# Optimization experiments

Measured on AMD Instinct MI355X. Metric: run time of the kernel, lower is better.

## Reference

```python
import jax, jax.numpy as jnp
from jax import lax
import numpy as np

C_IN, C_OUT, K, STRIDE, PAD = 64, 64, 3, 1, 1
EPS = 1e-5


def setup_inputs() -> dict:
    key = jax.random.key(0)
    ks = jax.random.split(key, 6)
    B, H, W = 4, 128, 128
    x = jax.random.normal(ks[0], (B, C_IN, H, W), jnp.float32)
    # small offset weights -> realistic sub-pixel offsets
    offset_w = jax.random.normal(ks[1], (2 * K * K, C_IN, K, K), jnp.float32) * 0.01
    offset_b = jax.random.normal(ks[2], (2 * K * K,), jnp.float32) * 0.01
    dcn_w = jax.random.normal(ks[3], (C_OUT, C_IN, K, K), jnp.float32) / np.sqrt(C_IN * K * K)
    gamma = jax.random.uniform(ks[4], (C_OUT,), jnp.float32, 0.5, 1.5)
    beta = jax.random.normal(ks[5], (C_OUT,), jnp.float32) * 0.1
    return dict(x=x, offset_w=offset_w, offset_b=offset_b, dcn_w=dcn_w, gamma=gamma, beta=beta)


def _bilinear_sample(xb, py, px):
    # xb: (C,H,W); py,px: (K2,Ho,Wo) absolute sample coords (may be out of bounds)
    H, W = xb.shape[1], xb.shape[2]
    y0 = jnp.floor(py); x0 = jnp.floor(px)
    wy = py - y0  # frac weights
    wx = px - x0

    def gather(yi, xi):
        yc = jnp.clip(yi, 0, H - 1).astype(jnp.int32)
        xc = jnp.clip(xi, 0, W - 1).astype(jnp.int32)
        v = xb[:, yc, xc]  # (C,K2,Ho,Wo)
        valid = ((yi >= 0) & (yi <= H - 1) & (xi >= 0) & (xi <= W - 1)).astype(xb.dtype)
        return v * valid[None]

    return (gather(y0, x0) * ((1 - wy) * (1 - wx))[None]
            + gather(y0, x0 + 1) * ((1 - wy) * wx)[None]
            + gather(y0 + 1, x0) * (wy * (1 - wx))[None]
            + gather(y0 + 1, x0 + 1) * (wy * wx)[None])  # (C,K2,Ho,Wo)


def reference(x, offset_w, offset_b, dcn_w, gamma, beta):
    B, C, H, W = x.shape
    K2 = K * K
    # offset conv (standard conv, NCHW)
    offset = lax.conv_general_dilated(
        x, offset_w, (STRIDE, STRIDE), [(PAD, PAD), (PAD, PAD)],
        dimension_numbers=("NCHW", "OIHW", "NCHW")) + offset_b[None, :, None, None]
    Ho, Wo = offset.shape[2], offset.shape[3]
    off = offset.reshape(B, K2, 2, Ho, Wo)  # interleaved (dy, dx) per tap
    dy, dx = off[:, :, 0], off[:, :, 1]
    # base sampling grid: out_pos*stride - pad + kernel tap index
    hs = (jnp.arange(Ho) * STRIDE - PAD).astype(x.dtype)
    ws = (jnp.arange(Wo) * STRIDE - PAD).astype(x.dtype)
    ki, kj = jnp.meshgrid(jnp.arange(K), jnp.arange(K), indexing="ij")
    ki = ki.reshape(K2).astype(x.dtype)
    kj = kj.reshape(K2).astype(x.dtype)
    py = dy + hs[None, None, :, None] + ki[None, :, None, None]  # (B,K2,Ho,Wo)
    px = dx + ws[None, None, None, :] + kj[None, :, None, None]

    sampled = jax.vmap(_bilinear_sample)(x, py, px)  # (B,C,K2,Ho,Wo)
    out = jnp.einsum("bckhw,ock->bohw", sampled, dcn_w.reshape(dcn_w.shape[0], C, K2))

    # BatchNorm (training-mode batch stats) + ReLU
    mean = out.mean((0, 2, 3))
    var = out.var((0, 2, 3))
    out = (out - mean[None, :, None, None]) * lax.rsqrt(var + EPS)[None, :, None, None]
    out = out * gamma[None, :, None, None] + beta[None, :, None, None]
    return jnp.maximum(out, 0.0)
```

## Files before the change

kernel.cpp:

```cpp
#include <hip/hip_runtime.h>

#define HW   16384
#define NPX  65536

typedef unsigned short u16;
typedef unsigned int   u32;
typedef short bf16x8 __attribute__((ext_vector_type(8)));
typedef float f32x4  __attribute__((ext_vector_type(4)));

__device__ __forceinline__ u16 f2b(float f) {
    u32 u = __float_as_uint(f);
    return (u16)((u + 0x7FFFu + ((u >> 16) & 1u)) >> 16);
}
__device__ __forceinline__ float blo(u32 u) { return __uint_as_float(u << 16); }
__device__ __forceinline__ float bhi(u32 u) { return __uint_as_float(u & 0xffff0000u); }

__device__ __forceinline__ u32 comb(u32 a00, u32 a01, u32 a10, u32 a11,
                                    float w00, float w01, float w10, float w11) {
    float lo = fmaf(w11, blo(a11), fmaf(w10, blo(a10), fmaf(w01, blo(a01), w00 * blo(a00))));
    float hi = fmaf(w11, bhi(a11), fmaf(w10, bhi(a10), fmaf(w01, bhi(a01), w00 * bhi(a00))));
    return ((__float_as_uint(lo) + 0x8000u) >> 16) | ((__float_as_uint(hi) + 0x8000u) & 0xffff0000u);
}
__device__ __forceinline__ bf16x8 comb4(int4 v00, int4 v01, int4 v10, int4 v11,
                                        float w00, float w01, float w10, float w11) {
    int4 r;
    r.x = comb(v00.x, v01.x, v10.x, v11.x, w00, w01, w10, w11);
    r.y = comb(v00.y, v01.y, v10.y, v11.y, w00, w01, w10, w11);
    r.z = comb(v00.z, v01.z, v10.z, v11.z, w00, w01, w10, w11);
    r.w = comb(v00.w, v01.w, v10.w, v11.w, w00, w01, w10, w11);
    return __builtin_bit_cast(bf16x8, r);
}

#define MFMA __builtin_amdgcn_mfma_f32_16x16x32_bf16

__global__ __launch_bounds__(256)
void k_pre(const float* __restrict__ x, const float* __restrict__ dw,
           const float* __restrict__ ow, u16* __restrict__ xh,
           u16* __restrict__ wtd, u16* __restrict__ wto,
           float* __restrict__ sums) {
    int tid = threadIdx.x;
    int bid = blockIdx.x;
    if (bid >= 512) {
        if (bid == 539) {
            for (int i = tid; i < 1024; i += 256) sums[i] = 0.f;
            return;
        }
        int gid = (bid - 512) * 256 + tid;
        if (gid >= 108 * 64) return;
        int fid = gid >> 6, lane = gid & 63;
        int mi = lane & 15, quad = lane >> 4;
        u32 w[4];
        if (fid < 72) {
            int tap = fid >> 3, rem = fid & 7;
            int ks = rem >> 2, nt = rem & 3;
            int n = nt * 16 + mi;
            int cb = ks * 32 + quad * 8;
#pragma unroll
            for (int i = 0; i < 4; ++i) {
                u32 lo = f2b(dw[(n * 64 + cb + 2 * i) * 9 + tap]);
                u32 hi = f2b(dw[(n * 64 + cb + 2 * i + 1) * 9 + tap]);
                w[i] = lo | (hi << 16);
            }
            *((int4*)wtd + (fid << 6) + lane) = make_int4(w[0], w[1], w[2], w[3]);
        } else {
            int f2 = fid - 72;
            int tap = f2 >> 2, rem = f2 & 3;
            int ks = rem >> 1, nt = rem & 1;
            int n = nt * 16 + mi;
            int cb = ks * 32 + quad * 8;
#pragma unroll
            for (int i = 0; i < 4; ++i) {
                u32 lo = (n < 18) ? f2b(ow[(n * 64 + cb + 2 * i) * 9 + tap]) : 0u;
                u32 hi = (n < 18) ? f2b(ow[(n * 64 + cb + 2 * i + 1) * 9 + tap]) : 0u;
                w[i] = lo | (hi << 16);
            }
            *((int4*)wto + (f2 << 6) + lane) = make_int4(w[0], w[1], w[2], w[3]);
        }
        return;
    }
    __shared__ u16 tile[64][138];
    int p0  = bid * 128;
    int b   = p0 >> 14;
    int hw0 = p0 & (HW - 1);
    int pxq = (tid & 31) * 4;
    int rr  = tid >> 5;
    const float* src = x + (size_t)b * 64 * HW + hw0 + pxq;
#pragma unroll
    for (int i = 0; i < 8; ++i) {
        int c = i * 8 + rr;
        float4 v = *(const float4*)(src + (size_t)c * HW);
        ushort4 h;
        h.x = f2b(v.x); h.y = f2b(v.y); h.z = f2b(v.z); h.w = f2b(v.w);
        *(ushort4*)&tile[c][pxq] = h;
    }
    __syncthreads();
    int sub = tid & 3;
#pragma unroll
    for (int j = 0; j < 2; ++j) {
        int px = j * 64 + (tid >> 2);
        u32 w[8];
#pragma unroll
        for (int t = 0; t < 8; ++t) {
            int c = sub * 16 + 2 * t;
            w[t] = (u32)tile[c][px] | ((u32)tile[c + 1][px] << 16);
        }
        u16* dst = xh + (size_t)(p0 + px) * 64 + sub * 16;
        *(int4*)dst       = make_int4(w[0], w[1], w[2], w[3]);
        *(int4*)(dst + 8) = make_int4(w[4], w[5], w[6], w[7]);
    }
}

__global__ __launch_bounds__(256, 4)
void k_main(const u16* __restrict__ xh, const u16* __restrict__ wto,
            const u16* __restrict__ wtd, const float* __restrict__ ob,
            float* __restrict__ out, float* __restrict__ sums) {
    __shared__ float offs[2][18][34];
    __shared__ float so[64][33];

    int tid = threadIdx.x;
    int vb  = (blockIdx.x & 7) * 256 + (blockIdx.x >> 3);
    int p0  = vb * 32;
    int b   = p0 >> 14;
    int hw0 = p0 & (HW - 1);
    int y   = hw0 >> 7;
    int x0  = hw0 & 127;
    int wave = tid >> 6, lane = tid & 63;
    int mi = lane & 15, quad = lane >> 4;
    int ks = wave >> 1;
    int m0 = (wave & 1) << 4;
    int xcol = x0 + m0 + mi;
    int koff = ks * 32 + quad * 8;
    const u16* xb = xh + (size_t)b * HW * 64;
    const bf16x8* WO = (const bf16x8*)wto;
    const bf16x8* WD = (const bf16x8*)wtd;

    int4 av[9];
#pragma unroll
    for (int tap = 0; tap < 9; ++tap) {
        int yy = y + tap / 3 - 1;
        int xx = xcol + tap % 3 - 1;
        int yc = min(max(yy, 0), 127), xc = min(max(xx, 0), 127);
        int4 a = *(const int4*)(xb + ((yc << 7) + xc) * 64 + koff);
        if (!(((unsigned)yy < 128u) && ((unsigned)xx < 128u)))
            a = make_int4(0, 0, 0, 0);
        av[tap] = a;
    }
    f32x4 oa0 = {0.f, 0.f, 0.f, 0.f}, oa1 = {0.f, 0.f, 0.f, 0.f};
#pragma unroll
    for (int tap = 0; tap < 9; ++tap) {
        bf16x8 af = __builtin_bit_cast(bf16x8, av[tap]);
        oa0 = MFMA(af, WO[((tap * 4 + ks * 2 + 0) << 6) + lane], oa0, 0, 0, 0);
        oa1 = MFMA(af, WO[((tap * 4 + ks * 2 + 1) << 6) + lane], oa1, 0, 0, 0);
    }
    {
        float bias0 = (ks == 0) ? ob[mi] : 0.f;
#pragma unroll
        for (int r = 0; r < 4; ++r)
            offs[ks][mi][m0 + quad * 4 + r] = oa0[r] + bias0;
        if (mi < 2) {
            float bias1 = (ks == 0) ? ob[16 + mi] : 0.f;
#pragma unroll
            for (int r = 0; r < 4; ++r)
                offs[ks][16 + mi][m0 + quad * 4 + r] = oa1[r] + bias1;
        }
    }
    __syncthreads();

    int pxl = m0 + mi;
    float offv[18];
#pragma unroll
    for (int m = 0; m < 18; ++m)
        offv[m] = offs[0][m][pxl] + offs[1][m][pxl];

    float fy = (float)y, fx = (float)xcol;
    auto coords = [&](int tap, float& w00, float& w01, float& w10, float& w11,
                      int& o00, int& o01, int& o10, int& o11) {
        float py  = offv[2 * tap]     + fy + (float)(tap / 3 - 1);
        float pf  = offv[2 * tap + 1] + fx + (float)(tap % 3 - 1);
        float y0f = floorf(py), x0f = floorf(pf);
        float wy  = py - y0f,   wx  = pf - x0f;
        int   iy0 = (int)y0f,   ix0 = (int)x0f;
        float vy0 = (y0f >=  0.f && y0f <= 127.f) ? 1.f : 0.f;
        float vy1 = (y0f >= -1.f && y0f <= 126.f) ? 1.f : 0.f;
        float vx0 = (x0f >=  0.f && x0f <= 127.f) ? 1.f : 0.f;
        float vx1 = (x0f >= -1.f && x0f <= 126.f) ? 1.f : 0.f;
        int cy0 = min(max(iy0, 0), 127), cy1 = min(max(iy0 + 1, 0), 127);
        int cx0 = min(max(ix0, 0), 127), cx1 = min(max(ix0 + 1, 0), 127);
        w00 = (1.f - wy) * (1.f - wx) * vy0 * vx0;
        w01 = (1.f - wy) * wx * vy0 * vx1;
        w10 = wy * (1.f - wx) * vy1 * vx0;
        w11 = wy * wx * vy1 * vx1;
        o00 = ((cy0 << 7) + cx0) * 64 + koff;
        o01 = ((cy0 << 7) + cx1) * 64 + koff;
        o10 = ((cy1 << 7) + cx0) * 64 + koff;
        o11 = ((cy1 << 7) + cx1) * 64 + koff;
    };

    f32x4 acc0 = {0.f,0.f,0.f,0.f}, acc1 = {0.f,0.f,0.f,0.f};
    f32x4 acc2 = {0.f,0.f,0.f,0.f}, acc3 = {0.f,0.f,0.f,0.f};

    float w00, w01, w10, w11;
    int   o00, o01, o10, o11;
    coords(0, w00, w01, w10, w11, o00, o01, o10, o11);
    int4 v00 = *(const int4*)(xb + o00);
    int4 v01 = *(const int4*)(xb + o01);
    int4 v10 = *(const int4*)(xb + o10);
    int4 v11 = *(const int4*)(xb + o11);
    bf16x8 b0 = WD[((ks * 4 + 0) << 6) + lane];
    bf16x8 b1 = WD[((ks * 4 + 1) << 6) + lane];
    bf16x8 b2 = WD[((ks * 4 + 2) << 6) + lane];
    bf16x8 b3 = WD[((ks * 4 + 3) << 6) + lane];

#pragma unroll
    for (int tap = 0; tap < 9; ++tap) {
        float nw00 = w00, nw01 = w01, nw10 = w10, nw11 = w11;
        int4 nv00 = v00, nv01 = v01, nv10 = v10, nv11 = v11;
        bf16x8 nb0 = b0, nb1 = b1, nb2 = b2, nb3 = b3;
        if (tap < 8) {
            int no00, no01, no10, no11;
            coords(tap + 1, nw00, nw01, nw10, nw11, no00, no01, no10, no11);
            nv00 = *(const int4*)(xb + no00);
            nv01 = *(const int4*)(xb + no01);
            nv10 = *(const int4*)(xb + no10);
            nv11 = *(const int4*)(xb + no11);
            nb0 = WD[(((tap + 1) * 8 + ks * 4 + 0) << 6) + lane];
            nb1 = WD[(((tap + 1) * 8 + ks * 4 + 1) << 6) + lane];
            nb2 = WD[(((tap + 1) * 8 + ks * 4 + 2) << 6) + lane];
            nb3 = WD[(((tap + 1) * 8 + ks * 4 + 3) << 6) + lane];
        }
        __builtin_amdgcn_sched_barrier(0);
        bf16x8 a = comb4(v00, v01, v10, v11, w00, w01, w10, w11);
        acc0 = MFMA(a, b0, acc0, 0, 0, 0);
        acc1 = MFMA(a, b1, acc1, 0, 0, 0);
        acc2 = MFMA(a, b2, acc2, 0, 0, 0);
        acc3 = MFMA(a, b3, acc3, 0, 0, 0);
        w00 = nw00; w01 = nw01; w10 = nw10; w11 = nw11;
        v00 = nv00; v01 = nv01; v10 = nv10; v11 = nv11;
        b0 = nb0; b1 = nb1; b2 = nb2; b3 = nb3;
    }

    if (ks == 1) {
#pragma unroll
        for (int r = 0; r < 4; ++r) {
            so[ 0 + mi][m0 + quad * 4 + r] = acc0[r];
            so[16 + mi][m0 + quad * 4 + r] = acc1[r];
            so[32 + mi][m0 + quad * 4 + r] = acc2[r];
            so[48 + mi][m0 + quad * 4 + r] = acc3[r];
        }
    }
    __syncthreads();
    if (ks == 0) {
#pragma unroll
        for (int r = 0; r < 4; ++r) {
            so[ 0 + mi][m0 + quad * 4 + r] += acc0[r];
            so[16 + mi][m0 + quad * 4 + r] += acc1[r];
            so[32 + mi][m0 + quad * 4 + r] += acc2[r];
            so[48 + mi][m0 + quad * 4 + r] += acc3[r];
        }
    }
    __syncthreads();

    int n  = tid >> 2;
    int c4 = tid & 3;
    int pl = c4 * 8;
    float s = 0.f, q = 0.f;
    float vals[8];
#pragma unroll
    for (int i = 0; i < 8; ++i) {
        float v = so[n][pl + i];
        vals[i] = v;
        s += v;
        q = fmaf(v, v, q);
    }
    float* dst = out + (size_t)(b * 64 + n) * HW + (y << 7) + x0 + pl;
    *(float4*)dst       = make_float4(vals[0], vals[1], vals[2], vals[3]);
    *(float4*)(dst + 4) = make_float4(vals[4], vals[5], vals[6], vals[7]);

    s += __shfl_xor(s, 1); s += __shfl_xor(s, 2);
    q += __shfl_xor(q, 1); q += __shfl_xor(q, 2);
    if (c4 == 0) {
        float* sb = sums + (blockIdx.x & 7) * 128;
        atomicAdd(&sb[n], s);
        atomicAdd(&sb[64 + n], q);
    }
}

__global__ __launch_bounds__(256)
void k_bn(float* __restrict__ out, const float* __restrict__ sums,
          const float* __restrict__ gamma, const float* __restrict__ beta) {
    int i4 = blockIdx.x * 256 + threadIdx.x;
    int e  = i4 << 2;
    int o  = (e >> 14) & 63;
    float sm = 0.f, sq = 0.f;
#pragma unroll
    for (int s8 = 0; s8 < 8; ++s8) {
        sm += sums[s8 * 128 + o];
        sq += sums[s8 * 128 + 64 + o];
    }
    const float n = 65536.f;
    float mean = sm / n;
    float var  = fmaxf(sq / n - mean * mean, 0.f);
    float sc   = rsqrtf(var + 1e-5f) * gamma[o];
    float sh   = beta[o] - mean * sc;
    float4 v = *(const float4*)&out[e];
    v.x = fmaxf(fmaf(v.x, sc, sh), 0.f);
    v.y = fmaxf(fmaf(v.y, sc, sh), 0.f);
    v.z = fmaxf(fmaf(v.z, sc, sh), 0.f);
    v.w = fmaxf(fmaf(v.w, sc, sh), 0.f);
    *(float4*)&out[e] = v;
}

extern "C" void kernel_launch(void* const* d_in, const int* in_sizes, int n_in,
                              void* d_out, int out_size, void* d_ws, size_t ws_size,
                              hipStream_t stream) {
    const float* x     = (const float*)d_in[0];
    const float* ow    = (const float*)d_in[1];
    const float* ob    = (const float*)d_in[2];
    const float* dw    = (const float*)d_in[3];
    const float* gamma = (const float*)d_in[4];
    const float* beta  = (const float*)d_in[5];
    float* out = (float*)d_out;
    char*  wsb = (char*)d_ws;
    u16*   xh   = (u16*)wsb;
    u16*   wtd  = (u16*)(wsb + 8388608);
    u16*   wto  = (u16*)(wsb + 8462336);
    float* sums = (float*)(wsb + 8499200);

    k_pre<<<540, 256, 0, stream>>>(x, dw, ow, xh, wtd, wto, sums);
    k_main<<<2048, 256, 0, stream>>>(xh, wto, wtd, ob, out, sums);
    k_bn<<<4096, 256, 0, stream>>>(out, sums, gamma, beta);
}
```

Baseline: 142.3 us.

## Batch gathers two taps at a time, raise occupancy, use perm for bf16 packing

Replaces the one-tap-ahead software prefetch with batches of two taps: the eight gathers for both taps are issued together, then combined and fed to MFMA. Weight fragments are no longer held in registers ahead of time and are read at their point of use. Launch bounds are raised to five blocks per SM to hide gather latency with more waves, and the two-bf16 pack becomes a single v_perm. The risks are register pressure under the tighter bound, possibly causing spills, and the loss of overlap between a batch's gathers and the previous batch's MFMAs.

```diff
diff --git a/kernel.cpp b/kernel.cpp
--- a/kernel.cpp
+++ b/kernel.cpp
@@ -19,7 +19,8 @@
                                     float w00, float w01, float w10, float w11) {
     float lo = fmaf(w11, blo(a11), fmaf(w10, blo(a10), fmaf(w01, blo(a01), w00 * blo(a00))));
     float hi = fmaf(w11, bhi(a11), fmaf(w10, bhi(a10), fmaf(w01, bhi(a01), w00 * bhi(a00))));
-    return ((__float_as_uint(lo) + 0x8000u) >> 16) | ((__float_as_uint(hi) + 0x8000u) & 0xffff0000u);
+    return __builtin_amdgcn_perm(__float_as_uint(hi) + 0x8000u,
+                                 __float_as_uint(lo) + 0x8000u, 0x07060302u);
 }
 __device__ __forceinline__ bf16x8 comb4(int4 v00, int4 v01, int4 v10, int4 v11,
                                         float w00, float w01, float w10, float w11) {
@@ -110,7 +111,7 @@
     }
 }
 
-__global__ __launch_bounds__(256, 4)
+__global__ __launch_bounds__(256, 5)
 void k_main(const u16* __restrict__ xh, const u16* __restrict__ wto,
             const u16* __restrict__ wtd, const float* __restrict__ ob,
             float* __restrict__ out, float* __restrict__ sums) {
@@ -173,70 +174,53 @@
         offv[m] = offs[0][m][pxl] + offs[1][m][pxl];
 
     float fy = (float)y, fx = (float)xcol;
-    auto coords = [&](int tap, float& w00, float& w01, float& w10, float& w11,
-                      int& o00, int& o01, int& o10, int& o11) {
-        float py  = offv[2 * tap]     + fy + (float)(tap / 3 - 1);
-        float pf  = offv[2 * tap + 1] + fx + (float)(tap % 3 - 1);
-        float y0f = floorf(py), x0f = floorf(pf);
-        float wy  = py - y0f,   wx  = pf - x0f;
-        int   iy0 = (int)y0f,   ix0 = (int)x0f;
-        float vy0 = (y0f >=  0.f && y0f <= 127.f) ? 1.f : 0.f;
-        float vy1 = (y0f >= -1.f && y0f <= 126.f) ? 1.f : 0.f;
-        float vx0 = (x0f >=  0.f && x0f <= 127.f) ? 1.f : 0.f;
-        float vx1 = (x0f >= -1.f && x0f <= 126.f) ? 1.f : 0.f;
-        int cy0 = min(max(iy0, 0), 127), cy1 = min(max(iy0 + 1, 0), 127);
-        int cx0 = min(max(ix0, 0), 127), cx1 = min(max(ix0 + 1, 0), 127);
-        w00 = (1.f - wy) * (1.f - wx) * vy0 * vx0;
-        w01 = (1.f - wy) * wx * vy0 * vx1;
-        w10 = wy * (1.f - wx) * vy1 * vx0;
-        w11 = wy * wx * vy1 * vx1;
-        o00 = ((cy0 << 7) + cx0) * 64 + koff;
-        o01 = ((cy0 << 7) + cx1) * 64 + koff;
-        o10 = ((cy1 << 7) + cx0) * 64 + koff;
-        o11 = ((cy1 << 7) + cx1) * 64 + koff;
-    };
-
     f32x4 acc0 = {0.f,0.f,0.f,0.f}, acc1 = {0.f,0.f,0.f,0.f};
     f32x4 acc2 = {0.f,0.f,0.f,0.f}, acc3 = {0.f,0.f,0.f,0.f};
 
-    float w00, w01, w10, w11;
-    int   o00, o01, o10, o11;
-    coords(0, w00, w01, w10, w11, o00, o01, o10, o11);
-    int4 v00 = *(const int4*)(xb + o00);
-    int4 v01 = *(const int4*)(xb + o01);
-    int4 v10 = *(const int4*)(xb + o10);
-    int4 v11 = *(const int4*)(xb + o11);
-    bf16x8 b0 = WD[((ks * 4 + 0) << 6) + lane];
-    bf16x8 b1 = WD[((ks * 4 + 1) << 6) + lane];
-    bf16x8 b2 = WD[((ks * 4 + 2) << 6) + lane];
-    bf16x8 b3 = WD[((ks * 4 + 3) << 6) + lane];
-
-#pragma unroll
-    for (int tap = 0; tap < 9; ++tap) {
-        float nw00 = w00, nw01 = w01, nw10 = w10, nw11 = w11;
-        int4 nv00 = v00, nv01 = v01, nv10 = v10, nv11 = v11;
-        bf16x8 nb0 = b0, nb1 = b1, nb2 = b2, nb3 = b3;
-        if (tap < 8) {
-            int no00, no01, no10, no11;
-            coords(tap + 1, nw00, nw01, nw10, nw11, no00, no01, no10, no11);
-            nv00 = *(const int4*)(xb + no00);
-            nv01 = *(const int4*)(xb + no01);
-            nv10 = *(const int4*)(xb + no10);
-            nv11 = *(const int4*)(xb + no11);
-            nb0 = WD[(((tap + 1) * 8 + ks * 4 + 0) << 6) + lane];
-            nb1 = WD[(((tap + 1) * 8 + ks * 4 + 1) << 6) + lane];
-            nb2 = WD[(((tap + 1) * 8 + ks * 4 + 2) << 6) + lane];
-            nb3 = WD[(((tap + 1) * 8 + ks * 4 + 3) << 6) + lane];
+#pragma unroll
+    for (int bt = 0; bt < 5; ++bt) {
+        const int ntap = (bt == 4) ? 1 : 2;
+        int4  vv[8];
+        float wts[2][4];
+#pragma unroll
+        for (int j = 0; j < 2; ++j) {
+            if (j < ntap) {
+                int tap = bt * 2 + j;
+                float py  = offv[2 * tap]     + fy + (float)(tap / 3 - 1);
+                float pf  = offv[2 * tap + 1] + fx + (float)(tap % 3 - 1);
+                float y0f = floorf(py), x0f = floorf(pf);
+                float wy  = py - y0f,   wx  = pf - x0f;
+                int   iy0 = (int)y0f,   ix0 = (int)x0f;
+                float vy0 = (y0f >=  0.f && y0f <= 127.f) ? 1.f : 0.f;
+                float vy1 = (y0f >= -1.f && y0f <= 126.f) ? 1.f : 0.f;
+                float vx0 = (x0f >=  0.f && x0f <= 127.f) ? 1.f : 0.f;
+                float vx1 = (x0f >= -1.f && x0f <= 126.f) ? 1.f : 0.f;
+                int cy0 = min(max(iy0, 0), 127), cy1 = min(max(iy0 + 1, 0), 127);
+                int cx0 = min(max(ix0, 0), 127), cx1 = min(max(ix0 + 1, 0), 127);
+                wts[j][0] = (1.f - wy) * (1.f - wx) * vy0 * vx0;
+                wts[j][1] = (1.f - wy) * wx * vy0 * vx1;
+                wts[j][2] = wy * (1.f - wx) * vy1 * vx0;
+                wts[j][3] = wy * wx * vy1 * vx1;
+                vv[j * 4 + 0] = *(const int4*)(xb + ((cy0 << 7) + cx0) * 64 + koff);
+                vv[j * 4 + 1] = *(const int4*)(xb + ((cy0 << 7) + cx1) * 64 + koff);
+                vv[j * 4 + 2] = *(const int4*)(xb + ((cy1 << 7) + cx0) * 64 + koff);
+                vv[j * 4 + 3] = *(const int4*)(xb + ((cy1 << 7) + cx1) * 64 + koff);
+            }
         }
         __builtin_amdgcn_sched_barrier(0);
-        bf16x8 a = comb4(v00, v01, v10, v11, w00, w01, w10, w11);
-        acc0 = MFMA(a, b0, acc0, 0, 0, 0);
-        acc1 = MFMA(a, b1, acc1, 0, 0, 0);
-        acc2 = MFMA(a, b2, acc2, 0, 0, 0);
-        acc3 = MFMA(a, b3, acc3, 0, 0, 0);
-        w00 = nw00; w01 = nw01; w10 = nw10; w11 = nw11;
-        v00 = nv00; v01 = nv01; v10 = nv10; v11 = nv11;
-        b0 = nb0; b1 = nb1; b2 = nb2; b3 = nb3;
+#pragma unroll
+        for (int j = 0; j < 2; ++j) {
+            if (j < ntap) {
+                int tap = bt * 2 + j;
+                bf16x8 a = comb4(vv[j * 4 + 0], vv[j * 4 + 1],
+                                 vv[j * 4 + 2], vv[j * 4 + 3],
+                                 wts[j][0], wts[j][1], wts[j][2], wts[j][3]);
+                acc0 = MFMA(a, WD[((tap * 8 + ks * 4 + 0) << 6) + lane], acc0, 0, 0, 0);
+                acc1 = MFMA(a, WD[((tap * 8 + ks * 4 + 1) << 6) + lane], acc1, 0, 0, 0);
+                acc2 = MFMA(a, WD[((tap * 8 + ks * 4 + 2) << 6) + lane], acc2, 0, 0, 0);
+                acc3 = MFMA(a, WD[((tap * 8 + ks * 4 + 3) << 6) + lane], acc3, 0, 0, 0);
+            }
+        }
     }
 
     if (ks == 1) {
```

New measurement: 147.2 us. 1.03x slower.
